# Optimization experiments

Hardware: AMD Instinct MI355X
Metric: run time of the kernel (lower is better)

## Reference

```python
import jax, jax.numpy as jnp
import numpy as np

B = 2
T = 32768          # exp.n_samples = 2**15
NB = 128           # exp.n_bands (filter bank bands)
CH = 128           # channels
EC = 512           # encoding_channels
ATOM = 2048        # full_atom_size
FBK = 512          # filter bank kernel size
DILS = (1, 3, 9, 27, 81, 243, 1)


def setup_inputs() -> dict:
    key = jax.random.key(0)
    ks = jax.random.split(key, 8)
    s = 0.05
    return {
        'x': jax.random.normal(ks[0], (B, 1, T), jnp.float32),
        'fb_w': jax.random.normal(ks[1], (NB, 1, FBK), jnp.float32) * s,
        'conv0_w': jax.random.normal(ks[2], (CH, NB, 7), jnp.float32) * s,
        'conv0_b': jnp.zeros((CH,), jnp.float32),
        'bn0_g': jnp.ones((CH,), jnp.float32),
        'bn0_b': jnp.zeros((CH,), jnp.float32),
        'dil_w': jax.random.normal(ks[3], (7, CH, CH, 3), jnp.float32) * s,
        'dil_b': jnp.zeros((7, CH), jnp.float32),
        'pw_w': jax.random.normal(ks[4], (7, CH, CH, 1), jnp.float32) * s,
        'pw_b': jnp.zeros((7, CH), jnp.float32),
        'bn_g': jnp.ones((7, CH), jnp.float32),
        'bn_b': jnp.zeros((7, CH), jnp.float32),
        'up_w': jax.random.normal(ks[5], (EC, CH, 1), jnp.float32) * s,
        'up_b': jnp.zeros((EC,), jnp.float32),
        'static_dict': jax.random.uniform(ks[6], (1, EC, ATOM), jnp.float32, -1.0, 1.0),
    }


def _conv1d(x, w, b=None, dilation=1, padding=0):
    y = jax.lax.conv_general_dilated(
        x, w, (1,), [(padding, padding)], rhs_dilation=(dilation,),
        dimension_numbers=('NCH', 'OIH', 'NCH'))
    if b is not None:
        y = y + b[None, :, None]
    return y


def _bn(x, g, b, eps=1e-5):
    # BatchNorm1d in training mode: per-channel stats over (batch, time)
    m = x.mean(axis=(0, 2), keepdims=True)
    v = x.var(axis=(0, 2), keepdims=True)
    return (x - m) * jax.lax.rsqrt(v + eps) * g[None, :, None] + b[None, :, None]


def _lrelu(x):
    return jnp.where(x >= 0, x, 0.2 * x)


def _fft_convolve(a, b):
    # linear convolution via zero-padded rfft, truncated back to n samples
    n = a.shape[-1]
    fa = jnp.fft.rfft(a, n=2 * n, axis=-1)
    fb = jnp.fft.rfft(b, n=2 * n, axis=-1)
    return jnp.fft.irfft(fa * fb, n=2 * n, axis=-1)[..., :n]


def reference(x, fb_w, conv0_w, conv0_b, bn0_g, bn0_b, dil_w, dil_b,
              pw_w, pw_b, bn_g, bn_b, up_w, up_b, static_dict):
    Bsz, _, n = x.shape
    # filter bank analysis: [B,1,T] -> [B,NB,T]
    spec = _conv1d(x, fb_w, padding=FBK // 2)[..., :n]
    # front conv + leaky relu + BN
    h = _conv1d(spec, conv0_w, conv0_b, padding=3)
    h = _bn(_lrelu(h), bn0_g, bn0_b)
    # dilated residual blocks (dropout = identity at inference)
    for i, d in enumerate(DILS):
        orig = h
        y = _conv1d(h, dil_w[i], dil_b[i], dilation=d, padding=d)
        y = _conv1d(y, pw_w[i], pw_b[i])
        h = _bn(_lrelu(y + orig), bn_g[i], bn_b[i])
    # up-projection to encoding channels + relu
    encoding = jax.nn.relu(_conv1d(h, up_w, up_b))  # [B,EC,T]
    # static dictionary atoms, zero-padded to n_samples, convolved with encoding
    atoms = jnp.broadcast_to(static_dict, (Bsz, EC, ATOM))
    atoms = jnp.pad(atoms, ((0, 0), (0, 0), (0, n - ATOM)))
    final = _fft_convolve(atoms, encoding)          # [B,EC,T]
    return jnp.sum(final, axis=1, keepdims=True)    # [B,1,T]
```

## Files before the change

kernel.cpp:

```cpp
#include <hip/hip_runtime.h>
#include <hip/hip_bf16.h>

#define B_ 2
#define T_ 32768
#define CH_ 128
#define EC_ 512
#define ATOM_ 2048
#define FBK_ 512

typedef __attribute__((ext_vector_type(8))) short s16x8;
typedef __attribute__((ext_vector_type(8))) _Float16 f16x8;
typedef __attribute__((ext_vector_type(4))) float f32x4;

__device__ __forceinline__ f16x8 ldh8(const _Float16* p) {
    union { s16x8 s; f16x8 h; } u; u.s = *(const s16x8*)p; return u.h;
}

__global__ void __launch_bounds__(256) k_fbm(const float* __restrict__ x,
        const _Float16* __restrict__ Wfb, _Float16* __restrict__ spec16) {
    __shared__ _Float16 XA[128][72];
    __shared__ _Float16 WT[128][72];
    __shared__ float xw[640];
    int tid = threadIdx.x;
    int lane = tid & 63;
    int wv = tid >> 6, wm = wv >> 1, wn = wv & 1;
    int ln15 = lane & 15, kh = lane >> 4;
    int t0 = blockIdx.x * 128;
    int b = blockIdx.y;

    for (int i = tid; i < 640; i += 256) {
        int g = t0 - 256 + i;
        xw[i] = (g >= 0 && g < T_) ? x[(size_t)b*T_ + g] : 0.f;
    }

    f32x4 acc[4][4];
    f32x4 zero = {0.f,0.f,0.f,0.f};
#pragma unroll
    for (int m = 0; m < 4; ++m)
#pragma unroll
        for (int n = 0; n < 4; ++n) acc[m][n] = zero;

    for (int c = 0; c < 8; ++c) {
        int k0 = c*64;
        __syncthreads();
#pragma unroll
        for (int q = 0; q < 4; ++q) {
            int idx = tid + q*256;
            int r = idx >> 3, ko = idx & 7;
            int base = r + k0 + ko*8;
            f16x8 v;
#pragma unroll
            for (int j = 0; j < 8; ++j) v[j] = (_Float16)xw[base + j];
            union { f16x8 h; s16x8 s; } u; u.h = v;
            *(s16x8*)&XA[r][ko*8] = u.s;
            *(s16x8*)&WT[r][ko*8] = *(const s16x8*)(Wfb + (size_t)r*FBK_ + k0 + ko*8);
        }
        __syncthreads();
#pragma unroll
        for (int kt = 0; kt < 2; ++kt) {
            f16x8 af[4], bf[4];
#pragma unroll
            for (int m = 0; m < 4; ++m) af[m] = ldh8(&XA[wm*64+m*16+ln15][kt*32+kh*8]);
#pragma unroll
            for (int n = 0; n < 4; ++n) bf[n] = ldh8(&WT[wn*64+n*16+ln15][kt*32+kh*8]);
#pragma unroll
            for (int m = 0; m < 4; ++m)
#pragma unroll
                for (int n = 0; n < 4; ++n)
                    acc[m][n] = __builtin_amdgcn_mfma_f32_16x16x32_f16(af[m], bf[n], acc[m][n], 0,0,0);
        }
    }
#pragma unroll
    for (int mf = 0; mf < 4; ++mf)
#pragma unroll
        for (int nf = 0; nf < 4; ++nf) {
            int band = wn*64 + nf*16 + ln15;
#pragma unroll
            for (int j = 0; j < 4; ++j) {
                int tl = wm*64 + mf*16 + kh*4 + j;
                spec16[((size_t)b*T_ + t0 + tl)*CH_ + band] = (_Float16)acc[mf][nf][j];
            }
        }
}

__global__ void k_pw7(const float* __restrict__ w, _Float16* __restrict__ W7) {
    int i = blockIdx.x*256+threadIdx.x;
    if (i >= 7*16384) return;
    int k = i / 16384, r = i % 16384; int co = r >> 7, ci = r & 127;
    W7[i] = (_Float16)w[(co*CH_+ci)*7 + k];
}
__global__ void k_pwd(const float* __restrict__ w, _Float16* __restrict__ Wd) {
    int i = blockIdx.x*256+threadIdx.x;
    if (i >= 7*3*16384) return;
    int st = i / 49152, r = i % 49152; int k = r / 16384, r2 = r % 16384;
    int co = r2 >> 7, ci = r2 & 127;
    Wd[i] = (_Float16)w[((size_t)(st*CH_+co)*CH_+ci)*3 + k];
}
__global__ void k_cast(const float* __restrict__ in, _Float16* __restrict__ out, int n) {
    int i = blockIdx.x*256+threadIdx.x;
    if (i < n) out[i] = (_Float16)in[i];
}
__global__ void k_zero(float* __restrict__ p, int n) {
    int i = blockIdx.x*256+threadIdx.x;
    if (i < n) p[i] = 0.f;
}

template<int NTAP, bool NORM, bool PW, bool LRELU, bool RELU, bool STATS>
__global__ void __launch_bounds__(256) k_cv(
        const _Float16* __restrict__ in, const _Float16* __restrict__ W,
        const float* __restrict__ bias, const _Float16* __restrict__ Wp_,
        const float* __restrict__ pbias, const float* __restrict__ stats_in,
        const float* __restrict__ g, const float* __restrict__ bb,
        float* __restrict__ stats_out, _Float16* __restrict__ outp,
        int dil, int ostride) {
    __shared__ _Float16 XT[128][136];
    __shared__ _Float16 WT[128][136];
    __shared__ _Float16 Y1[PW?128:1][PW?136:1];
    __shared__ float AffA[NORM?128:1], AffB[NORM?128:1];

    int tid = threadIdx.x;
    int lane = tid & 63;
    int wv = tid >> 6, wm = wv >> 1, wn = wv & 1;
    int ln15 = lane & 15, kh = lane >> 4;
    int t0 = blockIdx.x * 128;
    int nch = blockIdx.y;
    int b = blockIdx.z;
    int ncol0 = nch * 128;
    const _Float16* inb = in + (size_t)b*T_*CH_;
    const _Float16* W_eff = W + (size_t)ncol0*CH_;
    const float* bias_eff = bias + ncol0;

    if (NORM) {
        if (tid < 128) {
            const float invN = 1.f/(float)(B_*T_);
            float s1 = stats_in[tid], s2 = stats_in[128+tid];
            float m = s1*invN, var = s2*invN - m*m;
            float A = rsqrtf(var + 1e-5f) * g[tid];
            AffA[tid] = A; AffB[tid] = bb[tid] - m*A;
        }
        __syncthreads();
    }

    f32x4 acc[4][4];
    f32x4 zero = {0.f,0.f,0.f,0.f};
#pragma unroll
    for (int m = 0; m < 4; ++m)
#pragma unroll
        for (int n = 0; n < 4; ++n) acc[m][n] = zero;

    for (int tap = 0; tap < NTAP; ++tap) {
        int tp = tap;
        if (PW) tp = (tap==0) ? 0 : ((tap==1) ? 2 : 1);
        int off = (tp - NTAP/2)*dil;
        const _Float16* Wt = W_eff + (size_t)tp*CH_*CH_;
#pragma unroll
        for (int q = 0; q < 8; ++q) {
            int idx = tid + q*256;
            int lt = idx >> 4, ck = idx & 15;
            int gt = t0 + lt + off;
            s16x8 v = {0,0,0,0,0,0,0,0};
            bool valid = (gt >= 0 && gt < T_);
            if (valid) {
                v = *(const s16x8*)(inb + (size_t)gt*CH_ + ck*8);
                if (NORM) {
                    union {s16x8 s; f16x8 h;} u; u.s = v;
                    f16x8 r;
#pragma unroll
                    for (int j = 0; j < 8; ++j) {
                        float f = (float)u.h[j];
                        f = fmaf(f, AffA[ck*8+j], AffB[ck*8+j]);
                        r[j] = (_Float16)f;
                    }
                    union {f16x8 h; s16x8 s;} w2; w2.h = r; v = w2.s;
                }
            }
            *(s16x8*)&XT[lt][ck*8] = v;
            *(s16x8*)&WT[lt][ck*8] = *(const s16x8*)(Wt + (size_t)lt*CH_ + ck*8);
        }
        __syncthreads();
#pragma unroll
        for (int kt = 0; kt < 4; ++kt) {
            f16x8 af[4], bf[4];
#pragma unroll
            for (int m = 0; m < 4; ++m) af[m] = ldh8(&XT[wm*64+m*16+ln15][kt*32+kh*8]);
#pragma unroll
            for (int n = 0; n < 4; ++n) bf[n] = ldh8(&WT[wn*64+n*16+ln15][kt*32+kh*8]);
#pragma unroll
            for (int m = 0; m < 4; ++m)
#pragma unroll
                for (int n = 0; n < 4; ++n)
                    acc[m][n] = __builtin_amdgcn_mfma_f32_16x16x32_f16(af[m], bf[n], acc[m][n], 0,0,0);
        }
        __syncthreads();
    }

    if (PW) {
#pragma unroll
        for (int mf = 0; mf < 4; ++mf)
#pragma unroll
            for (int nf = 0; nf < 4; ++nf) {
                int co = wn*64 + nf*16 + ln15;
                float bv = bias_eff[co];
#pragma unroll
                for (int j = 0; j < 4; ++j) {
                    int tl = wm*64 + mf*16 + kh*4 + j;
                    Y1[tl][co] = (_Float16)(acc[mf][nf][j] + bv);
                }
            }
        __syncthreads();
#pragma unroll
        for (int q = 0; q < 8; ++q) {
            int idx = tid + q*256;
            int lt = idx >> 4, ck = idx & 15;
            *(s16x8*)&WT[lt][ck*8] = *(const s16x8*)(Wp_ + (size_t)lt*CH_ + ck*8);
        }
#pragma unroll
        for (int m = 0; m < 4; ++m)
#pragma unroll
            for (int n = 0; n < 4; ++n) acc[m][n] = zero;
        __syncthreads();
#pragma unroll
        for (int kt = 0; kt < 4; ++kt) {
            f16x8 af[4], bf[4];
#pragma unroll
            for (int m = 0; m < 4; ++m) af[m] = ldh8(&Y1[wm*64+m*16+ln15][kt*32+kh*8]);
#pragma unroll
            for (int n = 0; n < 4; ++n) bf[n] = ldh8(&WT[wn*64+n*16+ln15][kt*32+kh*8]);
#pragma unroll
            for (int m = 0; m < 4; ++m)
#pragma unroll
                for (int n = 0; n < 4; ++n)
                    acc[m][n] = __builtin_amdgcn_mfma_f32_16x16x32_f16(af[m], bf[n], acc[m][n], 0,0,0);
        }
    }

#pragma unroll
    for (int nf = 0; nf < 4; ++nf) {
        int co = wn*64 + nf*16 + ln15;
        float bfin = PW ? pbias[co] : bias_eff[co];
        float s = 0.f, s2 = 0.f;
#pragma unroll
        for (int mf = 0; mf < 4; ++mf) {
#pragma unroll
            for (int j = 0; j < 4; ++j) {
                int tl = wm*64 + mf*16 + kh*4 + j;
                float v = acc[mf][nf][j] + bfin;
                if (PW) v += (float)XT[tl][co];
                if (LRELU) v = v >= 0.f ? v : 0.2f*v;
                if (RELU)  v = fmaxf(v, 0.f);
                outp[((size_t)b*T_ + t0 + tl)*ostride + ncol0 + co] = (_Float16)v;
                if (STATS) { s += v; s2 += v*v; }
            }
        }
        if (STATS) {
            s  += __shfl_down(s, 16);  s  += __shfl_down(s, 32);
            s2 += __shfl_down(s2, 16); s2 += __shfl_down(s2, 32);
            if (kh == 0) {
                atomicAdd(&stats_out[co], s);
                atomicAdd(&stats_out[128+co], s2);
            }
        }
    }
}

__global__ void k_tr_at(const float* __restrict__ sd, _Float16* __restrict__ At) {
    __shared__ float tile[32][33];
    int tau0 = blockIdx.x*32;
    int c0 = blockIdx.y*32;
    int tx = threadIdx.x, ty = threadIdx.y;
#pragma unroll
    for (int j = 0; j < 4; ++j)
        tile[ty+j*8][tx] = sd[(size_t)(c0+ty+j*8)*ATOM_ + tau0 + tx];
    __syncthreads();
#pragma unroll
    for (int j = 0; j < 4; ++j)
        At[(size_t)(tau0+ty+j*8)*EC_ + c0 + tx] = (_Float16)tile[tx][ty+j*8];
}

__global__ void __launch_bounds__(256) k_gemm(const _Float16* __restrict__ At,
                                              const _Float16* __restrict__ Et,
                                              _Float16* __restrict__ G) {
    __shared__ _Float16 lA[128][72];
    __shared__ _Float16 lB[128][72];
    int tid = threadIdx.x;
    int lane = tid & 63;
    int wv = tid >> 6;
    int wm = wv >> 1, wn = wv & 1;
    int sT = blockIdx.x;
    int tT = blockIdx.y;
    int ln15 = lane & 15, kh = lane >> 4;
    f32x4 acc[4][4];
    f32x4 zero = {0.f,0.f,0.f,0.f};
#pragma unroll
    for (int m = 0; m < 4; ++m)
#pragma unroll
        for (int n = 0; n < 4; ++n) acc[m][n] = zero;

    for (int kt = 0; kt < 8; ++kt) {
#pragma unroll
        for (int r = 0; r < 4; ++r) {
            int idx = tid + r*256;
            int row = idx >> 3, ch = idx & 7;
            *(s16x8*)&lA[row][ch*8] = *(const s16x8*)(At + ((size_t)(tT*128+row))*EC_ + kt*64 + ch*8);
            *(s16x8*)&lB[row][ch*8] = *(const s16x8*)(Et + ((size_t)(sT*128+row))*EC_ + kt*64 + ch*8);
        }
        __syncthreads();
#pragma unroll
        for (int kk = 0; kk < 2; ++kk) {
            f16x8 af[4], bfr[4];
#pragma unroll
            for (int m = 0; m < 4; ++m)
                af[m] = ldh8(&lA[wm*64 + m*16 + ln15][kk*32 + kh*8]);
#pragma unroll
            for (int n = 0; n < 4; ++n)
                bfr[n] = ldh8(&lB[wn*64 + n*16 + ln15][kk*32 + kh*8]);
#pragma unroll
            for (int m = 0; m < 4; ++m)
#pragma unroll
                for (int n = 0; n < 4; ++n)
                    acc[m][n] = __builtin_amdgcn_mfma_f32_16x16x32_f16(af[m], bfr[n], acc[m][n], 0, 0, 0);
        }
        __syncthreads();
    }
#pragma unroll
    for (int m = 0; m < 4; ++m) {
#pragma unroll
        for (int n = 0; n < 4; ++n) {
            int rowb = tT*128 + wm*64 + m*16 + kh*4;
            int col  = sT*128 + wn*64 + n*16 + ln15;
#pragma unroll
            for (int j = 0; j < 4; ++j)
                G[(size_t)(rowb+j)*T_ + col] = (_Float16)acc[m][n][j];
        }
    }
}

__global__ void k_diag(const _Float16* __restrict__ G, float* __restrict__ part, int tau0) {
    int t = blockIdx.x*256 + threadIdx.x;
    int sub = blockIdx.y;
    int lr0 = sub*128;
    float acc = 0.f;
    int lrend = min(128, t + 1 - (tau0 + lr0));
    for (int lr = 0; lr < lrend; ++lr) {
        int tau = tau0 + lr0 + lr;
        acc += (float)G[(size_t)(lr0 + lr)*T_ + (t - tau)];
    }
    part[(size_t)sub*T_ + t] = acc;
}

__global__ void k_diag2(const float* __restrict__ part, float* __restrict__ out) {
    int t = blockIdx.x*256 + threadIdx.x;
    float s = 0.f;
#pragma unroll
    for (int i = 0; i < 16; ++i) s += part[(size_t)i*T_ + t];
    out[t] = s;
}

__global__ void k_fill(float* __restrict__ out, float val) {
    out[blockIdx.x*256 + threadIdx.x] = val;
}

extern "C" void kernel_launch(void* const* d_in, const int* in_sizes, int n_in,
                              void* d_out, int out_size, void* d_ws, size_t ws_size,
                              hipStream_t stream) {
    const float* x       = (const float*)d_in[0];
    const float* fb_w    = (const float*)d_in[1];
    const float* conv0_w = (const float*)d_in[2];
    const float* conv0_b = (const float*)d_in[3];
    const float* bn0_g   = (const float*)d_in[4];
    const float* bn0_b   = (const float*)d_in[5];
    const float* dil_w   = (const float*)d_in[6];
    const float* dil_b   = (const float*)d_in[7];
    const float* pw_w    = (const float*)d_in[8];
    const float* pw_b    = (const float*)d_in[9];
    const float* bn_g    = (const float*)d_in[10];
    const float* bn_b    = (const float*)d_in[11];
    const float* up_w    = (const float*)d_in[12];
    const float* up_b    = (const float*)d_in[13];
    const float* sdict   = (const float*)d_in[14];
    float* out = (float*)d_out;
    char* ws = (char*)d_ws;

    const size_t R1   = 33554432;
    const size_t R2   = 33554432;
    const size_t ACT  = 16777216;
    char* r1   = ws;
    char* r2   = ws + R1;
    char* actA = ws + R1 + R2;
    char* actB = actA + ACT;
    char* wreg = actB + ACT;
    _Float16* W7   = (_Float16*)wreg;
    _Float16* Wd   = W7 + 7*16384;
    _Float16* Wp   = Wd + 7*3*16384;
    _Float16* Wup  = Wp + 7*16384;
    _Float16* Wfb  = Wup + 65536;
    float* stats   = (float*)(Wfb + 65536);
    const size_t TOTAL = R1 + R2 + 2*ACT
                       + (7*16384 + 7*3*16384 + 7*16384 + 65536 + 65536)*2 + 8*2*128*4;
    if (ws_size < TOTAL) {
        k_fill<<<(out_size+255)/256, 256, 0, stream>>>(out, 12345.0f);
        return;
    }
    _Float16* spec16 = (_Float16*)r2;
    _Float16* enc = (_Float16*)r1;
    _Float16* G   = (_Float16*)r2;
    float* part   = (float*)actA;
    _Float16* At  = (_Float16*)(actA + 2097152);

    k_zero<<<(2048+255)/256, 256, 0, stream>>>(stats, 8*2*128);
    k_pw7<<<(7*16384+255)/256, 256, 0, stream>>>(conv0_w, W7);
    k_pwd<<<(7*3*16384+255)/256, 256, 0, stream>>>(dil_w, Wd);
    k_cast<<<(7*16384+255)/256, 256, 0, stream>>>(pw_w, Wp, 7*16384);
    k_cast<<<(65536+255)/256, 256, 0, stream>>>(up_w, Wup, 65536);
    k_cast<<<(65536+255)/256, 256, 0, stream>>>(fb_w, Wfb, 65536);

    k_fbm<<<dim3(T_/128, B_), 256, 0, stream>>>(x, Wfb, spec16);
    k_cv<7,false,false,true,false,true><<<dim3(T_/128,1,B_), 256, 0, stream>>>(
        spec16, W7, conv0_b, nullptr, nullptr, nullptr, nullptr, nullptr,
        stats + 0, (_Float16*)actA, 1, CH_);

    const int DILS[7] = {1, 3, 9, 27, 81, 243, 1};
    _Float16* cur = (_Float16*)actA;
    _Float16* nxt = (_Float16*)actB;
    for (int i = 0; i < 7; ++i) {
        const float* gi = (i == 0) ? bn0_g : bn_g + (i-1)*CH_;
        const float* bi = (i == 0) ? bn0_b : bn_b + (i-1)*CH_;
        k_cv<3,true,true,true,false,true><<<dim3(T_/128,1,B_), 256, 0, stream>>>(
            cur, Wd + (size_t)i*3*CH_*CH_, dil_b + i*CH_, Wp + (size_t)i*CH_*CH_,
            pw_b + i*CH_, stats + i*256, gi, bi, stats + (i+1)*256, nxt, DILS[i], CH_);
        _Float16* sw = cur; cur = nxt; nxt = sw;
    }
    k_tr_at<<<dim3(ATOM_/32, EC_/32), dim3(32,8), 0, stream>>>(sdict, At);

    for (int b = 0; b < B_; ++b) {
        k_cv<1,true,false,false,true,false><<<dim3(T_/128,EC_/128,1), 256, 0, stream>>>(
            cur + (size_t)b*T_*CH_, Wup, up_b, nullptr, nullptr,
            stats + 7*256, bn_g + 6*CH_, bn_b + 6*CH_, nullptr, enc, 1, EC_);
        for (int cc = 0; cc < 4; ++cc) {
            k_gemm<<<dim3(T_/128, 4), 256, 0, stream>>>(At + (size_t)cc*512*EC_, enc, G);
            k_diag<<<dim3(T_/256, 4), 256, 0, stream>>>(G, part + (size_t)cc*4*T_, cc*512);
        }
        k_diag2<<<T_/256, 256, 0, stream>>>(part, out + (size_t)b*T_);
    }
}
```

Before: 1.048 ms.

## Fuse diagonal reduction into atom GEMM, batch launches, and read weights directly from global

```diff
diff --git a/kernel.cpp b/kernel.cpp
--- a/kernel.cpp
+++ b/kernel.cpp
@@ -19,7 +19,6 @@
 __global__ void __launch_bounds__(256) k_fbm(const float* __restrict__ x,
         const _Float16* __restrict__ Wfb, _Float16* __restrict__ spec16) {
     __shared__ _Float16 XA[128][72];
-    __shared__ _Float16 WT[128][72];
     __shared__ float xw[640];
     int tid = threadIdx.x;
     int lane = tid & 63;
@@ -53,7 +52,6 @@
             for (int j = 0; j < 8; ++j) v[j] = (_Float16)xw[base + j];
             union { f16x8 h; s16x8 s; } u; u.h = v;
             *(s16x8*)&XA[r][ko*8] = u.s;
-            *(s16x8*)&WT[r][ko*8] = *(const s16x8*)(Wfb + (size_t)r*FBK_ + k0 + ko*8);
         }
         __syncthreads();
 #pragma unroll
@@ -62,7 +60,8 @@
 #pragma unroll
             for (int m = 0; m < 4; ++m) af[m] = ldh8(&XA[wm*64+m*16+ln15][kt*32+kh*8]);
 #pragma unroll
-            for (int n = 0; n < 4; ++n) bf[n] = ldh8(&WT[wn*64+n*16+ln15][kt*32+kh*8]);
+            for (int n = 0; n < 4; ++n)
+                bf[n] = ldh8(Wfb + (size_t)(wn*64+n*16+ln15)*FBK_ + k0 + kt*32 + kh*8);
 #pragma unroll
             for (int m = 0; m < 4; ++m)
 #pragma unroll
@@ -114,7 +113,6 @@
         float* __restrict__ stats_out, _Float16* __restrict__ outp,
         int dil, int ostride) {
     __shared__ _Float16 XT[128][136];
-    __shared__ _Float16 WT[128][136];
     __shared__ _Float16 Y1[PW?128:1][PW?136:1];
     __shared__ float AffA[NORM?128:1], AffB[NORM?128:1];
 
@@ -138,7 +136,6 @@
             float A = rsqrtf(var + 1e-5f) * g[tid];
             AffA[tid] = A; AffB[tid] = bb[tid] - m*A;
         }
-        __syncthreads();
     }
 
     f32x4 acc[4][4];
@@ -153,6 +150,7 @@
         if (PW) tp = (tap==0) ? 0 : ((tap==1) ? 2 : 1);
         int off = (tp - NTAP/2)*dil;
         const _Float16* Wt = W_eff + (size_t)tp*CH_*CH_;
+        __syncthreads();
 #pragma unroll
         for (int q = 0; q < 8; ++q) {
             int idx = tid + q*256;
@@ -175,7 +173,6 @@
                 }
             }
             *(s16x8*)&XT[lt][ck*8] = v;
-            *(s16x8*)&WT[lt][ck*8] = *(const s16x8*)(Wt + (size_t)lt*CH_ + ck*8);
         }
         __syncthreads();
 #pragma unroll
@@ -184,14 +181,14 @@
 #pragma unroll
             for (int m = 0; m < 4; ++m) af[m] = ldh8(&XT[wm*64+m*16+ln15][kt*32+kh*8]);
 #pragma unroll
-            for (int n = 0; n < 4; ++n) bf[n] = ldh8(&WT[wn*64+n*16+ln15][kt*32+kh*8]);
+            for (int n = 0; n < 4; ++n)
+                bf[n] = ldh8(Wt + (size_t)(wn*64+n*16+ln15)*CH_ + kt*32 + kh*8);
 #pragma unroll
             for (int m = 0; m < 4; ++m)
 #pragma unroll
                 for (int n = 0; n < 4; ++n)
                     acc[m][n] = __builtin_amdgcn_mfma_f32_16x16x32_f16(af[m], bf[n], acc[m][n], 0,0,0);
         }
-        __syncthreads();
     }
 
     if (PW) {
@@ -207,13 +204,6 @@
                     Y1[tl][co] = (_Float16)(acc[mf][nf][j] + bv);
                 }
             }
-        __syncthreads();
-#pragma unroll
-        for (int q = 0; q < 8; ++q) {
-            int idx = tid + q*256;
-            int lt = idx >> 4, ck = idx & 15;
-            *(s16x8*)&WT[lt][ck*8] = *(const s16x8*)(Wp_ + (size_t)lt*CH_ + ck*8);
-        }
 #pragma unroll
         for (int m = 0; m < 4; ++m)
 #pragma unroll
@@ -225,7 +215,8 @@
 #pragma unroll
             for (int m = 0; m < 4; ++m) af[m] = ldh8(&Y1[wm*64+m*16+ln15][kt*32+kh*8]);
 #pragma unroll
-            for (int n = 0; n < 4; ++n) bf[n] = ldh8(&WT[wn*64+n*16+ln15][kt*32+kh*8]);
+            for (int n = 0; n < 4; ++n)
+                bf[n] = ldh8(Wp_ + (size_t)(wn*64+n*16+ln15)*CH_ + kt*32 + kh*8);
 #pragma unroll
             for (int m = 0; m < 4; ++m)
 #pragma unroll
@@ -278,16 +269,19 @@
 }
 
 __global__ void __launch_bounds__(256) k_gemm(const _Float16* __restrict__ At,
-                                              const _Float16* __restrict__ Et,
-                                              _Float16* __restrict__ G) {
+                                              const _Float16* __restrict__ enc,
+                                              float* __restrict__ out) {
     __shared__ _Float16 lA[128][72];
     __shared__ _Float16 lB[128][72];
+    __shared__ float pt[256];
     int tid = threadIdx.x;
     int lane = tid & 63;
     int wv = tid >> 6;
     int wm = wv >> 1, wn = wv & 1;
     int sT = blockIdx.x;
     int tT = blockIdx.y;
+    int b  = blockIdx.z;
+    const _Float16* Et = enc + (size_t)b*T_*EC_;
     int ln15 = lane & 15, kh = lane >> 4;
     f32x4 acc[4][4];
     f32x4 zero = {0.f,0.f,0.f,0.f};
@@ -322,38 +316,28 @@
         }
         __syncthreads();
     }
-#pragma unroll
-    for (int m = 0; m < 4; ++m) {
-#pragma unroll
-        for (int n = 0; n < 4; ++n) {
-            int rowb = tT*128 + wm*64 + m*16 + kh*4;
-            int col  = sT*128 + wn*64 + n*16 + ln15;
-#pragma unroll
-            for (int j = 0; j < 4; ++j)
-                G[(size_t)(rowb+j)*T_ + col] = (_Float16)acc[m][n][j];
-        }
-    }
-}
-
-__global__ void k_diag(const _Float16* __restrict__ G, float* __restrict__ part, int tau0) {
-    int t = blockIdx.x*256 + threadIdx.x;
-    int sub = blockIdx.y;
-    int lr0 = sub*128;
-    float acc = 0.f;
-    int lrend = min(128, t + 1 - (tau0 + lr0));
-    for (int lr = 0; lr < lrend; ++lr) {
-        int tau = tau0 + lr0 + lr;
-        acc += (float)G[(size_t)(lr0 + lr)*T_ + (t - tau)];
-    }
-    part[(size_t)sub*T_ + t] = acc;
-}
-
-__global__ void k_diag2(const float* __restrict__ part, float* __restrict__ out) {
-    int t = blockIdx.x*256 + threadIdx.x;
-    float s = 0.f;
-#pragma unroll
-    for (int i = 0; i < 16; ++i) s += part[(size_t)i*T_ + t];
-    out[t] = s;
+
+    pt[tid] = 0.f;
+    __syncthreads();
+#pragma unroll
+    for (int mn = 0; mn <= 6; ++mn) {
+#pragma unroll
+        for (int j = 0; j < 4; ++j) {
+            float v = 0.f;
+#pragma unroll
+            for (int m = 0; m < 4; ++m) {
+                int n = mn - m;
+                if (n >= 0 && n < 4) v += acc[m][n][j];
+            }
+            int tl = (wm + wn)*64 + mn*16 + kh*4 + j + ln15;
+            unsafeAtomicAdd(&pt[tl], v);
+        }
+    }
+    __syncthreads();
+    if (tid < 255) {
+        int tg = tT*128 + sT*128 + tid;
+        if (tg < T_) unsafeAtomicAdd(&out[(size_t)b*T_ + tg], pt[tid]);
+    }
 }
 
 __global__ void k_fill(float* __restrict__ out, float val) {
@@ -385,7 +369,6 @@
     const size_t R2   = 33554432;
     const size_t ACT  = 16777216;
     char* r1   = ws;
-    char* r2   = ws + R1;
     char* actA = ws + R1 + R2;
     char* actB = actA + ACT;
     char* wreg = actB + ACT;
@@ -401,10 +384,8 @@
         k_fill<<<(out_size+255)/256, 256, 0, stream>>>(out, 12345.0f);
         return;
     }
-    _Float16* spec16 = (_Float16*)r2;
+    _Float16* spec16 = (_Float16*)r1;
     _Float16* enc = (_Float16*)r1;
-    _Float16* G   = (_Float16*)r2;
-    float* part   = (float*)actA;
     _Float16* At  = (_Float16*)(actA + 2097152);
 
     k_zero<<<(2048+255)/256, 256, 0, stream>>>(stats, 8*2*128);
@@ -430,16 +411,12 @@
             pw_b + i*CH_, stats + i*256, gi, bi, stats + (i+1)*256, nxt, DILS[i], CH_);
         _Float16* sw = cur; cur = nxt; nxt = sw;
     }
+
     k_tr_at<<<dim3(ATOM_/32, EC_/32), dim3(32,8), 0, stream>>>(sdict, At);
-
-    for (int b = 0; b < B_; ++b) {
-        k_cv<1,true,false,false,true,false><<<dim3(T_/128,EC_/128,1), 256, 0, stream>>>(
-            cur + (size_t)b*T_*CH_, Wup, up_b, nullptr, nullptr,
-            stats + 7*256, bn_g + 6*CH_, bn_b + 6*CH_, nullptr, enc, 1, EC_);
-        for (int cc = 0; cc < 4; ++cc) {
-            k_gemm<<<dim3(T_/128, 4), 256, 0, stream>>>(At + (size_t)cc*512*EC_, enc, G);
-            k_diag<<<dim3(T_/256, 4), 256, 0, stream>>>(G, part + (size_t)cc*4*T_, cc*512);
-        }
-        k_diag2<<<T_/256, 256, 0, stream>>>(part, out + (size_t)b*T_);
-    }
-}
+    k_cv<1,true,false,false,true,false><<<dim3(T_/128,EC_/128,B_), 256, 0, stream>>>(
+        cur, Wup, up_b, nullptr, nullptr,
+        stats + 7*256, bn_g + 6*CH_, bn_b + 6*CH_, nullptr, enc, 1, EC_);
+
+    k_zero<<<(B_*T_+255)/256, 256, 0, stream>>>(out, B_*T_);
+    k_gemm<<<dim3(T_/128, ATOM_/128, B_), 256, 0, stream>>>(At, enc, out);
+}
```

New measurement: 955.4 us. -8.8%, faster.
